# Kernel tuning notes

Measured on AMD Instinct MI355X. Metric: run time of the kernel, lower is better.

## Reference

```python
import jax, jax.numpy as jnp
import numpy as np

BATCH, INPUT_SIZE, ALPHA_DIM = 512, 64, 64


def fast_logexpmv(A, B):
    """Log-semiring matmul: C[b,i,j] = logsumexp_k A[b,i,k] + B[b,k,j], numerically stable."""
    a_max = jnp.max(A, axis=-1, keepdims=True)   # (B, i, 1)
    b_max = jnp.max(B, axis=-2, keepdims=True)   # (B, 1, j)
    C = jnp.log(jnp.matmul(jnp.exp(A - a_max), jnp.exp(B - b_max)))
    return C + a_max + b_max


def setup_inputs() -> dict:
    key = jax.random.key(0)
    k1, k2, k3 = jax.random.split(key, 3)
    x = jax.random.bernoulli(k1, 0.5, (BATCH, INPUT_SIZE)).astype(jnp.float32)
    theta = jax.random.uniform(k2, (1, INPUT_SIZE, ALPHA_DIM, ALPHA_DIM), dtype=jnp.float32)
    u_log_p_alpha = jax.random.normal(k3, (1, INPUT_SIZE - 1, 1, ALPHA_DIM), dtype=jnp.float32)
    return {"x": x, "theta": theta, "u_log_p_alpha": u_log_p_alpha}


def reference(x, theta, u_log_p_alpha):
    # normalized log p(alpha) over last dim (matches _log_p_alpha's manual logsumexp)
    log_p_alpha = jax.nn.log_softmax(u_log_p_alpha, axis=-1)          # (1, T-1, 1, a)
    # per-position Bernoulli log-likelihood matrices:
    # -clamp(theta,0) + theta*x - log(1 + exp(-|theta|))  -> (B, T, a, a)
    log_px_mats = (-jnp.clip(theta, 0.0)
                   + theta * x[:, :, None, None]
                   - jnp.log1p(jnp.exp(-jnp.abs(theta))))
    joint = log_px_mats[:, :-1] + log_p_alpha                          # (B, T-1, a, a)
    mats = jnp.transpose(joint, (1, 0, 2, 3))                          # (T-1, B, a, a)

    def step(carry, m):
        return fast_logexpmv(carry, m), None

    left, _ = jax.lax.scan(step, mats[0], mats[1:])                    # (B, a, a)
    p_xn_g_alpha_n1 = log_px_mats[:, -1, :, 0:1]                       # (B, a, 1)
    log_px = fast_logexpmv(left, p_xn_g_alpha_n1)                      # (B, a, 1)
    return log_px
```

## Files before the change

kernel.cpp:

```cpp
#include <hip/hip_runtime.h>
#include <hip/hip_bf16.h>


#define NSTEP 63

typedef __attribute__((ext_vector_type(8)))  short short8;
typedef __attribute__((ext_vector_type(16))) float f32x16;

union U8 { short8 v; unsigned u[4]; unsigned short s[8]; };

static __device__ __forceinline__ unsigned short bf16b(float f) {
  union { __hip_bfloat16 h; unsigned short u; } cv;
  cv.h = __float2bfloat16(f);
  return cv.u;
}
static __device__ __forceinline__ unsigned pack2(float a, float b) {
  return (unsigned)bf16b(a) | ((unsigned)bf16b(b) << 16);
}
static __device__ __forceinline__ float bfcvt(unsigned short s) {
  return __uint_as_float((unsigned)s << 16);
}

__global__ __launch_bounds__(256) void e_kernel(
    const float* __restrict__ theta, const float* __restrict__ ulpa,
    unsigned short* __restrict__ EA, unsigned short* __restrict__ EB) {
  int t = blockIdx.x;
  int tid = threadIdx.x;
  __shared__ float sig[64][65];
  __shared__ float pa[64];

  if (tid < 64) {
    float u = ulpa[t * 64 + tid];
    float m = u;
    #pragma unroll
    for (int o = 32; o >= 1; o >>= 1) m = fmaxf(m, __shfl_xor(m, o));
    float e = __expf(u - m);
    float s = e;
    #pragma unroll
    for (int o = 32; o >= 1; o >>= 1) s += __shfl_xor(s, o);
    pa[tid] = e / s;
  }

  const float4* th4 = (const float4*)(theta + t * 4096);
  #pragma unroll
  for (int k = 0; k < 4; ++k) {
    int i = tid + k * 256;
    float4 v = th4[i];
    int m = i >> 4, n0 = (i & 15) * 4;
    sig[m][n0 + 0] = 1.0f / (1.0f + __expf(-v.x));
    sig[m][n0 + 1] = 1.0f / (1.0f + __expf(-v.y));
    sig[m][n0 + 2] = 1.0f / (1.0f + __expf(-v.z));
    sig[m][n0 + 3] = 1.0f / (1.0f + __expf(-v.w));
  }
  __syncthreads();

  unsigned short* EA0 = EA + (size_t)(t * 2 + 0) * 4096;
  unsigned short* EA1 = EA + (size_t)(t * 2 + 1) * 4096;
  unsigned short* EB0 = EB + (size_t)(t * 2 + 0) * 4096;
  unsigned short* EB1 = EB + (size_t)(t * 2 + 1) * 4096;

  #pragma unroll
  for (int k = 0; k < 4; ++k) {
    int i = tid + k * 256;
    int m = i >> 4, n0 = (i & 15) * 4;
    float p0 = pa[n0], p1 = pa[n0 + 1], p2 = pa[n0 + 2], p3 = pa[n0 + 3];
    float s0 = sig[m][n0], s1 = sig[m][n0 + 1];
    float s2 = sig[m][n0 + 2], s3 = sig[m][n0 + 3];
    *reinterpret_cast<uint2*>(&EA1[m * 64 + n0]) =
        make_uint2(pack2(s0 * p0, s1 * p1), pack2(s2 * p2, s3 * p3));
    *reinterpret_cast<uint2*>(&EA0[m * 64 + n0]) =
        make_uint2(pack2((1.0f - s0) * p0, (1.0f - s1) * p1),
                   pack2((1.0f - s2) * p2, (1.0f - s3) * p3));
  }
  #pragma unroll
  for (int k = 0; k < 4; ++k) {
    int i = tid + k * 256;
    int n = i >> 4, m0 = (i & 15) * 4;
    float pn = pa[n];
    float s0 = sig[m0][n], s1 = sig[m0 + 1][n];
    float s2 = sig[m0 + 2][n], s3 = sig[m0 + 3][n];
    *reinterpret_cast<uint2*>(&EB1[n * 64 + m0]) =
        make_uint2(pack2(s0 * pn, s1 * pn), pack2(s2 * pn, s3 * pn));
    *reinterpret_cast<uint2*>(&EB0[n * 64 + m0]) =
        make_uint2(pack2((1.0f - s0) * pn, (1.0f - s1) * pn),
                   pack2((1.0f - s2) * pn, (1.0f - s3) * pn));
  }
}

static __device__ __forceinline__ void mm64(const short8 A[4][2],
                                            const short8 B[4][2],
                                            f32x16 C[2][2]) {
  #pragma unroll
  for (int ti = 0; ti < 2; ++ti)
    #pragma unroll
    for (int j = 0; j < 2; ++j)
      #pragma unroll
      for (int r = 0; r < 16; ++r) C[ti][j][r] = 0.0f;
  #pragma unroll
  for (int kc = 0; kc < 4; ++kc)
    #pragma unroll
    for (int j = 0; j < 2; ++j)
      #pragma unroll
      for (int ti = 0; ti < 2; ++ti)
        C[ti][j] = __builtin_amdgcn_mfma_f32_32x32x16_bf16(
            A[kc][ti], B[kc][j], C[ti][j], 0, 0, 0);
}

static __device__ __forceinline__ void loadA_g(short8 A[4][2],
                                               const unsigned short* M,
                                               int lo, int hi) {
  #pragma unroll
  for (int kc = 0; kc < 4; ++kc)
    #pragma unroll
    for (int ti = 0; ti < 2; ++ti)
      A[kc][ti] = *reinterpret_cast<const short8*>(
          &M[(32 * ti + lo) * 64 + 16 * kc + 8 * hi]);
}
static __device__ __forceinline__ void loadB_g(short8 B[4][2],
                                               const unsigned short* M,
                                               int lo, int hi) {
  #pragma unroll
  for (int kc = 0; kc < 4; ++kc)
    #pragma unroll
    for (int j = 0; j < 2; ++j)
      B[kc][j] = *reinterpret_cast<const short8*>(
          &M[(32 * j + lo) * 64 + 16 * kc + 8 * hi]);
}

static __device__ __forceinline__ void store_role0(const f32x16 C[2][2],
                                                   char* base, int lo, int hi) {
  #pragma unroll
  for (int ti = 0; ti < 2; ++ti)
    #pragma unroll
    for (int j = 0; j < 2; ++j)
      #pragma unroll
      for (int r = 0; r < 16; ++r) {
        int m = 32 * ti + (r & 3) + 8 * (r >> 2) + 4 * hi;
        int n = 32 * j + lo;
        unsigned byteoff =
            ((unsigned)(m * 128 + n * 2)) ^ ((unsigned)(m & 7) << 4);
        *reinterpret_cast<unsigned short*>(base + byteoff) = bf16b(C[ti][j][r]);
      }
}

static __device__ __forceinline__ void loadA_lds(short8 A[4][2],
                                                 const char* base,
                                                 int lo, int hi) {
  #pragma unroll
  for (int kc = 0; kc < 4; ++kc)
    #pragma unroll
    for (int ti = 0; ti < 2; ++ti) {
      int m = 32 * ti + lo;
      unsigned byteoff = ((unsigned)(m * 128 + (16 * kc + 8 * hi) * 2)) ^
                         ((unsigned)(m & 7) << 4);
      A[kc][ti] = *reinterpret_cast<const short8*>(base + byteoff);
    }
}

static __device__ __forceinline__ void rebuildB(const f32x16 C[2][2],
                                                short8 B[4][2], int hi) {
  #pragma unroll
  for (int kc = 0; kc < 4; ++kc) {
    int Me = 2 * kc, Mo = 2 * kc + 1;
    int tie = Me >> 2, me = Me & 3;
    int tio = Mo >> 2, mo = Mo & 3;
    #pragma unroll
    for (int j = 0; j < 2; ++j) {
      unsigned pe0 = pack2(C[tie][j][4 * me + 0], C[tie][j][4 * me + 1]);
      unsigned pe1 = pack2(C[tie][j][4 * me + 2], C[tie][j][4 * me + 3]);
      unsigned po0 = pack2(C[tio][j][4 * mo + 0], C[tio][j][4 * mo + 1]);
      unsigned po1 = pack2(C[tio][j][4 * mo + 2], C[tio][j][4 * mo + 3]);
      unsigned s0 = hi ? pe0 : po0;
      unsigned s1 = hi ? pe1 : po1;
      unsigned r0 = (unsigned)__shfl_xor((int)s0, 32);
      unsigned r1 = (unsigned)__shfl_xor((int)s1, 32);
      U8 f;
      f.u[0] = hi ? r0 : pe0;
      f.u[1] = hi ? r1 : pe1;
      f.u[2] = hi ? po0 : r0;
      f.u[3] = hi ? po1 : r1;
      B[kc][j] = f.v;
    }
  }
}

__global__ __launch_bounds__(64) void quad_kernel(
    const unsigned short* __restrict__ EA, const unsigned short* __restrict__ EB,
    unsigned short* __restrict__ MqC) {
  __shared__ __align__(16) char Lsh[8192];

  int bid = blockIdx.x;
  int lane = threadIdx.x, lo = lane & 31, hi = lane >> 5;
  int v, nt, t0;
  if (bid < 240) { v = bid & 15; nt = 4; t0 = 4 * (bid >> 4); }
  else           { v = bid - 240; nt = 3; t0 = 60; }

  short8 A[4][2], B[4][2];
  f32x16 C1[2][2], C2[2][2], C3[2][2];

  if (nt == 4) {
    int b0 = v & 1, b1 = (v >> 1) & 1, b2 = (v >> 2) & 1, b3 = (v >> 3) & 1;
    loadA_g(A, EB + (size_t)((t0 + 3) * 2 + b3) * 4096, lo, hi);
    loadB_g(B, EA + (size_t)((t0 + 2) * 2 + b2) * 4096, lo, hi);
    mm64(A, B, C1);
    loadA_g(A, EB + (size_t)((t0 + 1) * 2 + b1) * 4096, lo, hi);
    loadB_g(B, EA + (size_t)((t0 + 0) * 2 + b0) * 4096, lo, hi);
    mm64(A, B, C2);
    store_role0(C1, Lsh, lo, hi);
    loadA_lds(A, Lsh, lo, hi);
    rebuildB(C2, B, hi);
    mm64(A, B, C3);
  } else {
    int b0 = v & 1, b1 = (v >> 1) & 1, b2 = (v >> 2) & 1;
    loadA_g(A, EB + (size_t)((t0 + 2) * 2 + b2) * 4096, lo, hi);
    loadB_g(B, EA + (size_t)((t0 + 1) * 2 + b1) * 4096, lo, hi);
    mm64(A, B, C1);
    store_role0(C1, Lsh, lo, hi);
    loadA_lds(A, Lsh, lo, hi);
    loadB_g(B, EA + (size_t)((t0 + 0) * 2 + b0) * 4096, lo, hi);
    mm64(A, B, C3);
  }

  unsigned short* outp = MqC + (size_t)bid * 4096;
  #pragma unroll
  for (int ti = 0; ti < 2; ++ti)
    #pragma unroll
    for (int j = 0; j < 2; ++j)
      #pragma unroll
      for (int r = 0; r < 16; ++r) {
        int m = 32 * ti + (r & 3) + 8 * (r >> 2) + 4 * hi;
        int n = 32 * j + lo;
        outp[(m >> 3) * 512 + n * 8 + (m & 7)] = bf16b(C3[ti][j][r]);
      }
}

__global__ __launch_bounds__(64) void chain_kernel(
    const float* __restrict__ x, const float* __restrict__ theta,
    const unsigned short* __restrict__ MqC, float* __restrict__ out) {
  int b = blockIdx.x;
  int lane = threadIdx.x;

  unsigned long long mask = __ballot(x[b * 64 + lane] != 0.0f);

  __shared__ __align__(16) float u_lds[64];

  float th = theta[63 * 4096 + lane * 64];
  float sg = 1.0f / (1.0f + __expf(-th));
  float u = ((mask >> 63) & 1ull) ? sg : (1.0f - sg);
  float acc = 0.0f;

#define GIDX(g) ((g) < 15 ? (g) * 16 + (int)((mask >> (4 * (g))) & 15ull) \
                          : 240 + (int)((mask >> 60) & 7ull))

  short8 qa[8], qb[8], qc[8];

#define PRE(REG, PG)                                                      \
  {                                                                       \
    const unsigned short* Pb = MqC + (size_t)GIDX(PG) * 4096 + lane * 8;  \
    _Pragma("unroll")                                                     \
    for (int gi = 0; gi < 8; ++gi)                                        \
      REG[gi] = *reinterpret_cast<const short8*>(Pb + gi * 512);          \
  }

#define STEP(QREG, PG, PREG)                                              \
  {                                                                       \
    u_lds[lane] = u;                                                      \
    if ((PG) >= 0) PRE(PREG, PG);                                         \
    float s0 = 0.f, s1 = 0.f, s2 = 0.f, s3 = 0.f;                         \
    _Pragma("unroll")                                                     \
    for (int gi = 0; gi < 8; ++gi) {                                      \
      U8 f; f.v = QREG[gi];                                               \
      float4 uu0 = *(const float4*)&u_lds[gi * 8];                        \
      float4 uu1 = *(const float4*)&u_lds[gi * 8 + 4];                    \
      s0 = fmaf(bfcvt(f.s[0]), uu0.x, s0);                                \
      s1 = fmaf(bfcvt(f.s[1]), uu0.y, s1);                                \
      s2 = fmaf(bfcvt(f.s[2]), uu0.z, s2);                                \
      s3 = fmaf(bfcvt(f.s[3]), uu0.w, s3);                                \
      s0 = fmaf(bfcvt(f.s[4]), uu1.x, s0);                                \
      s1 = fmaf(bfcvt(f.s[5]), uu1.y, s1);                                \
      s2 = fmaf(bfcvt(f.s[6]), uu1.z, s2);                                \
      s3 = fmaf(bfcvt(f.s[7]), uu1.w, s3);                                \
    }                                                                     \
    u = (s0 + s1) + (s2 + s3);                                            \
  }

  PRE(qa, 15);
  PRE(qb, 14);

  STEP(qa, 13, qc);
  STEP(qb, 12, qa);
  STEP(qc, 11, qb);
  STEP(qa, 10, qc);
  STEP(qb,  9, qa);
  STEP(qc,  8, qb);
  STEP(qa,  7, qc);
  STEP(qb,  6, qa);

  {
    float m = u;
    #pragma unroll
    for (int o = 32; o >= 1; o >>= 1) m = fmaxf(m, __shfl_xor(m, o));
    acc += __logf(m);
    u *= (1.0f / m);
  }

  STEP(qc,  5, qb);
  STEP(qa,  4, qc);
  STEP(qb,  3, qa);
  STEP(qc,  2, qb);
  STEP(qa,  1, qc);
  STEP(qb,  0, qa);
  STEP(qc, -1, qb);
  STEP(qa, -1, qb);

#undef STEP
#undef PRE
#undef GIDX

  out[b * 64 + lane] = logf(u) + acc;
}

extern "C" void kernel_launch(void* const* d_in, const int* in_sizes, int n_in,
                              void* d_out, int out_size, void* d_ws, size_t ws_size,
                              hipStream_t stream) {
  const float* x     = (const float*)d_in[0];
  const float* theta = (const float*)d_in[1];
  const float* ulpa  = (const float*)d_in[2];
  float* out = (float*)d_out;

  unsigned short* MqC = (unsigned short*)d_ws;
  unsigned short* EA  = MqC + (size_t)248 * 4096;
  unsigned short* EB  = EA + (size_t)NSTEP * 2 * 4096;

  hipLaunchKernelGGL(e_kernel, dim3(NSTEP), dim3(256), 0, stream,
                     theta, ulpa, EA, EB);
  hipLaunchKernelGGL(quad_kernel, dim3(248), dim3(64), 0, stream,
                     EA, EB, MqC);
  hipLaunchKernelGGL(chain_kernel, dim3(512), dim3(64), 0, stream,
                     x, theta, MqC, out);
}
```

Baseline: 76.12 us.

## Split chain matvec across four waves with cross-lane reduction per step

The chain kernel now uses 256 threads per batch row instead of 64. Each lane handles 16 of the 64 k-terms for one output element, and the partial sums are combined with two xor shuffles. The state vector is double-buffered in LDS, with a block barrier after every step. This shortens each thread's serial FMA chain and per-thread register footprint. The cost is a __syncthreads per step and more threads, and the rescale is folded into a multiplier applied at the next step.

```diff
diff --git a/kernel.cpp b/kernel.cpp
--- a/kernel.cpp
+++ b/kernel.cpp
@@ -234,90 +234,113 @@
       }
 }
 
-__global__ __launch_bounds__(64) void chain_kernel(
+__global__ __launch_bounds__(256) void chain_kernel(
     const float* __restrict__ x, const float* __restrict__ theta,
     const unsigned short* __restrict__ MqC, float* __restrict__ out) {
   int b = blockIdx.x;
-  int lane = threadIdx.x;
-
-  unsigned long long mask = __ballot(x[b * 64 + lane] != 0.0f);
-
-  __shared__ __align__(16) float u_lds[64];
-
-  float th = theta[63 * 4096 + lane * 64];
+  int tid = threadIdx.x;
+  int w = tid >> 6, l = tid & 63;
+  int al = l & 15;
+  int q = l >> 4;
+  int a = 16 * w + al;
+
+  unsigned long long mask = __ballot(x[b * 64 + l] != 0.0f);
+
+  __shared__ __align__(16) float ubuf[2][64];
+
+  float th = theta[63 * 4096 + l * 64];
   float sg = 1.0f / (1.0f + __expf(-th));
-  float u = ((mask >> 63) & 1ull) ? sg : (1.0f - sg);
-  float acc = 0.0f;
+  float pv = ((mask >> 63) & 1ull) ? sg : (1.0f - sg);
+  if (w == 0) ubuf[0][l] = pv;
+  __syncthreads();
 
 #define GIDX(g) ((g) < 15 ? (g) * 16 + (int)((mask >> (4 * (g))) & 15ull) \
                           : 240 + (int)((mask >> 60) & 7ull))
 
-  short8 qa[8], qb[8], qc[8];
-
-#define PRE(REG, PG)                                                      \
-  {                                                                       \
-    const unsigned short* Pb = MqC + (size_t)GIDX(PG) * 4096 + lane * 8;  \
-    _Pragma("unroll")                                                     \
-    for (int gi = 0; gi < 8; ++gi)                                        \
-      REG[gi] = *reinterpret_cast<const short8*>(Pb + gi * 512);          \
-  }
-
-#define STEP(QREG, PG, PREG)                                              \
-  {                                                                       \
-    u_lds[lane] = u;                                                      \
-    if ((PG) >= 0) PRE(PREG, PG);                                         \
-    float s0 = 0.f, s1 = 0.f, s2 = 0.f, s3 = 0.f;                         \
-    _Pragma("unroll")                                                     \
-    for (int gi = 0; gi < 8; ++gi) {                                      \
-      U8 f; f.v = QREG[gi];                                               \
-      float4 uu0 = *(const float4*)&u_lds[gi * 8];                        \
-      float4 uu1 = *(const float4*)&u_lds[gi * 8 + 4];                    \
-      s0 = fmaf(bfcvt(f.s[0]), uu0.x, s0);                                \
-      s1 = fmaf(bfcvt(f.s[1]), uu0.y, s1);                                \
-      s2 = fmaf(bfcvt(f.s[2]), uu0.z, s2);                                \
-      s3 = fmaf(bfcvt(f.s[3]), uu0.w, s3);                                \
-      s0 = fmaf(bfcvt(f.s[4]), uu1.x, s0);                                \
-      s1 = fmaf(bfcvt(f.s[5]), uu1.y, s1);                                \
-      s2 = fmaf(bfcvt(f.s[6]), uu1.z, s2);                                \
-      s3 = fmaf(bfcvt(f.s[7]), uu1.w, s3);                                \
-    }                                                                     \
-    u = (s0 + s1) + (s2 + s3);                                            \
+  short8 qa[2], qb[2], qc[2];
+
+#define PRE(REG, PG)                                                        \
+  {                                                                         \
+    const unsigned short* Pb =                                              \
+        MqC + (size_t)GIDX(PG) * 4096 + (q * 1024 + a * 8);                 \
+    REG[0] = *reinterpret_cast<const short8*>(Pb);                          \
+    REG[1] = *reinterpret_cast<const short8*>(Pb + 512);                    \
+  }
+
+  float rscale = 1.0f, acc = 0.0f;
+
+#define STEP(QREG, PG, PREG, CUR, DO_RS, LAST)                              \
+  {                                                                         \
+    if ((PG) >= 0) PRE(PREG, PG);                                           \
+    const float* uc = ubuf[CUR];                                            \
+    float4 u0 = *(const float4*)&uc[16 * q + 0];                            \
+    float4 u1 = *(const float4*)&uc[16 * q + 4];                            \
+    float4 u2 = *(const float4*)&uc[16 * q + 8];                            \
+    float4 u3 = *(const float4*)&uc[16 * q + 12];                           \
+    U8 f0, f1;                                                              \
+    f0.v = QREG[0]; f1.v = QREG[1];                                         \
+    float s0 = 0.f, s1 = 0.f, s2 = 0.f, s3 = 0.f;                           \
+    s0 = fmaf(bfcvt(f0.s[0]), u0.x, s0);                                    \
+    s1 = fmaf(bfcvt(f0.s[1]), u0.y, s1);                                    \
+    s2 = fmaf(bfcvt(f0.s[2]), u0.z, s2);                                    \
+    s3 = fmaf(bfcvt(f0.s[3]), u0.w, s3);                                    \
+    s0 = fmaf(bfcvt(f0.s[4]), u1.x, s0);                                    \
+    s1 = fmaf(bfcvt(f0.s[5]), u1.y, s1);                                    \
+    s2 = fmaf(bfcvt(f0.s[6]), u1.z, s2);                                    \
+    s3 = fmaf(bfcvt(f0.s[7]), u1.w, s3);                                    \
+    s0 = fmaf(bfcvt(f1.s[0]), u2.x, s0);                                    \
+    s1 = fmaf(bfcvt(f1.s[1]), u2.y, s1);                                    \
+    s2 = fmaf(bfcvt(f1.s[2]), u2.z, s2);                                    \
+    s3 = fmaf(bfcvt(f1.s[3]), u2.w, s3);                                    \
+    s0 = fmaf(bfcvt(f1.s[4]), u3.x, s0);                                    \
+    s1 = fmaf(bfcvt(f1.s[5]), u3.y, s1);                                    \
+    s2 = fmaf(bfcvt(f1.s[6]), u3.z, s2);                                    \
+    s3 = fmaf(bfcvt(f1.s[7]), u3.w, s3);                                    \
+    float s = (s0 + s1) + (s2 + s3);                                        \
+    s += __shfl_xor(s, 16);                                                 \
+    s += __shfl_xor(s, 32);                                                 \
+    if (DO_RS) s *= rscale;                                                 \
+    if (LAST) {                                                             \
+      if (q == 0) out[b * 64 + a] = logf(s) + acc;                          \
+    } else {                                                                \
+      if (q == 0) ubuf[(CUR) ^ 1][a] = s;                                   \
+      __syncthreads();                                                      \
+    }                                                                       \
   }
 
   PRE(qa, 15);
   PRE(qb, 14);
 
-  STEP(qa, 13, qc);
-  STEP(qb, 12, qa);
-  STEP(qc, 11, qb);
-  STEP(qa, 10, qc);
-  STEP(qb,  9, qa);
-  STEP(qc,  8, qb);
-  STEP(qa,  7, qc);
-  STEP(qb,  6, qa);
+  STEP(qa, 13, qc, 0, 0, 0);
+  STEP(qb, 12, qa, 1, 0, 0);
+  STEP(qc, 11, qb, 0, 0, 0);
+  STEP(qa, 10, qc, 1, 0, 0);
+  STEP(qb,  9, qa, 0, 0, 0);
+  STEP(qc,  8, qb, 1, 0, 0);
+  STEP(qa,  7, qc, 0, 0, 0);
+  STEP(qb,  6, qa, 1, 0, 0);
 
   {
-    float m = u;
+    float uv = ubuf[0][l];
+    float m = uv;
     #pragma unroll
     for (int o = 32; o >= 1; o >>= 1) m = fmaxf(m, __shfl_xor(m, o));
-    acc += __logf(m);
-    u *= (1.0f / m);
-  }
-
-  STEP(qc,  5, qb);
-  STEP(qa,  4, qc);
-  STEP(qb,  3, qa);
-  STEP(qc,  2, qb);
-  STEP(qa,  1, qc);
-  STEP(qb,  0, qa);
-  STEP(qc, -1, qb);
-  STEP(qa, -1, qb);
+    rscale = 1.0f / m;
+    acc = __logf(m);
+  }
+
+  STEP(qc,  5, qb, 0, 1, 0);
+  STEP(qa,  4, qc, 1, 0, 0);
+  STEP(qb,  3, qa, 0, 0, 0);
+  STEP(qc,  2, qb, 1, 0, 0);
+  STEP(qa,  1, qc, 0, 0, 0);
+  STEP(qb,  0, qa, 1, 0, 0);
+  STEP(qc, -1, qb, 0, 0, 0);
+  STEP(qa, -1, qb, 1, 0, 1);
 
 #undef STEP
 #undef PRE
 #undef GIDX
-
-  out[b * 64 + lane] = logf(u) + acc;
 }
 
 extern "C" void kernel_launch(void* const* d_in, const int* in_sizes, int n_in,
@@ -336,6 +359,6 @@
                      theta, ulpa, EA, EB);
   hipLaunchKernelGGL(quad_kernel, dim3(248), dim3(64), 0, stream,
                      EA, EB, MqC);
-  hipLaunchKernelGGL(chain_kernel, dim3(512), dim3(64), 0, stream,
+  hipLaunchKernelGGL(chain_kernel, dim3(512), dim3(256), 0, stream,
                      x, theta, MqC, out);
 }
```

Measured after the change: 73.80 us, median of 2. 1.03x faster.
